# Optimization experiments

Hardware: AMD Instinct MI355X
Metric: run time of the kernel (lower is better)

## Reference

```python
import jax, jax.numpy as jnp
import numpy as np

N, D = 65536, 64            # flattened batch, state dim (size_in)
G, K = 4, 512               # number of gammas, components per gamma


def setup_inputs() -> dict:
    key = jax.random.key(0)
    k1, k2 = jax.random.split(key)
    states = jax.random.normal(k1, (N, D), dtype=jnp.float32)
    centers = jax.random.normal(k2, (G, K, D), dtype=jnp.float32)  # RBF centers, one bank per gamma
    gammas = jnp.array([0.5, 1.0, 2.0, 5.0], dtype=jnp.float32)
    return {"states": states, "centers": centers, "gammas": gammas}


def reference(states, centers, gammas):
    # states: [N, D]; centers: [G, K, D]; gammas: [G]
    x2 = jnp.sum(states * states, axis=-1)            # [N]
    c2 = jnp.sum(centers * centers, axis=-1)          # [G, K]
    xc = jnp.einsum('nd,gkd->gnk', states, centers)   # [G, N, K]
    d2 = x2[None, :, None] + c2[:, None, :] - 2.0 * xc  # [G, N, K]
    d2 = jnp.maximum(d2, 0.0)
    feats = jnp.exp(-gammas[:, None, None] * d2)      # [G, N, K]
    # concatenate per-gamma feature banks along feature dim -> [N, G*K]
    out = jnp.moveaxis(feats, 0, 1).reshape(states.shape[0], -1)
    return out
```

## Files before the change

### kernel.cpp

```cpp
#include <hip/hip_runtime.h>
#include <math.h>

#define N_TOT 65536
#define D_DIM 64
#define G_NUM 4
#define K_NUM 512
#define RB    256

typedef __attribute__((ext_vector_type(4))) float  f32x4;
typedef __attribute__((ext_vector_type(8))) short  short8;

typedef const __attribute__((address_space(1))) void glb_cv;
typedef __attribute__((address_space(3))) void lds_v;

__device__ __forceinline__ unsigned int f2u(float x)        { return __builtin_bit_cast(unsigned int, x); }
__device__ __forceinline__ float        u2f(unsigned int x) { return __builtin_bit_cast(float, x); }

__device__ __forceinline__ unsigned int bf_rne(float x) {
    unsigned int u = f2u(x);
    return (u + 0x7FFFu + ((u >> 16) & 1u)) >> 16;
}

__device__ __forceinline__ int swz(int row, int byteInRow) {
    return (row << 7) + (byteInRow ^ ((row & 7) << 4));
}

__global__ void prep_kernel(const float* __restrict__ in,
                            unsigned char* __restrict__ tiles,
                            float* __restrict__ sq, int nrows)
{
    int gtid = blockIdx.x * 256 + threadIdx.x;
    if (gtid >= nrows * 8) return;
    int row = gtid >> 3, c = gtid & 7;
    const float* p = in + (size_t)row * D_DIM + 8 * c;
    float4 v0 = *(const float4*)p;
    float4 v1 = *(const float4*)(p + 4);
    float vs[8] = {v0.x, v0.y, v0.z, v0.w, v1.x, v1.y, v1.z, v1.w};
    unsigned hi[4], lo[4];
    float s = 0.f;
    #pragma unroll
    for (int i = 0; i < 4; ++i) {
        float a = vs[2 * i], b = vs[2 * i + 1];
        s += a * a + b * b;
        unsigned ha = f2u(a) & 0xFFFF0000u, hb = f2u(b) & 0xFFFF0000u;
        hi[i] = (ha >> 16) | hb;
        lo[i] = bf_rne(a - u2f(ha)) | (bf_rne(b - u2f(hb)) << 16);
    }
    int tile = row >> 7, r = row & 127;
    int cs = c ^ (r & 7);
    unsigned char* base = tiles + (size_t)tile * 32768 + r * 128 + cs * 16;
    *(uint4*)(base)         = make_uint4(hi[0], hi[1], hi[2], hi[3]);
    *(uint4*)(base + 16384) = make_uint4(lo[0], lo[1], lo[2], lo[3]);
    s += __shfl_xor(s, 1, 64);
    s += __shfl_xor(s, 2, 64);
    s += __shfl_xor(s, 4, 64);
    if (c == 0) sq[row] = s;
}

__global__ __launch_bounds__(512, 2)
void rbf_mfma3(const unsigned char* __restrict__ Aprep,
               const unsigned char* __restrict__ Bprep,
               const float* __restrict__ gammas,
               const float* __restrict__ x2,
               const float* __restrict__ c2,
               float* __restrict__ out)
{
    __shared__ __align__(16) unsigned char lds[131072];

    const int tid  = threadIdx.x;
    const int lane = tid & 63;
    const int w    = tid >> 6;
    const int n0   = blockIdx.x * RB;

    const unsigned char* Asrc = Aprep + (size_t)blockIdx.x * 65536;
    #pragma unroll
    for (int i = 0; i < 8; ++i) {
        const int off = i * 8192 + w * 1024;
        __builtin_amdgcn_global_load_lds((glb_cv*)(Asrc + off + lane * 16),
                                         (lds_v*)(lds + off), 16, 0, 0);
    }
    #pragma unroll
    for (int i = 0; i < 4; ++i) {
        const int off = i * 8192 + w * 1024;
        __builtin_amdgcn_global_load_lds((glb_cv*)(Bprep + off + lane * 16),
                                         (lds_v*)(lds + 65536 + off), 16, 0, 0);
    }
    __syncthreads();

    const int wrow = w >> 1;
    const int wcol = w & 1;
    const int fr   = lane & 15;
    const int q    = lane >> 4;

    short8 xhi[4][2], xlo[4][2];
    #pragma unroll
    for (int ms = 0; ms < 4; ++ms) {
        const int row = wrow * 64 + ms * 16 + fr;
        const int base = (row >> 7) * 32768;
        #pragma unroll
        for (int h = 0; h < 2; ++h) {
            const int off = base + swz(row & 127, 64 * h + 16 * q);
            xhi[ms][h] = *(const short8*)(lds + off);
            xlo[ms][h] = *(const short8*)(lds + off + 16384);
        }
    }

    float x2v[4];
    #pragma unroll
    for (int ms = 0; ms < 4; ++ms)
        x2v[ms] = x2[n0 + wrow * 64 + ms * 16 + fr];

    const float4 gm = *(const float4*)gammas;

    #pragma unroll 1
    for (int t = 0; t < 16; ++t) {
        const int g  = t >> 2;
        const int kt = t & 3;
        const int bb = 65536 + (t & 1) * 32768;

        if (t < 15) {
            const unsigned char* Bsrc = Bprep + (size_t)(t + 1) * 32768;
            const int dstb = 65536 + ((t + 1) & 1) * 32768;
            #pragma unroll
            for (int i = 0; i < 4; ++i) {
                const int off = i * 8192 + w * 1024;
                __builtin_amdgcn_global_load_lds((glb_cv*)(Bsrc + off + lane * 16),
                                                 (lds_v*)(lds + dstb + off), 16, 0, 0);
            }
        }

        f32x4 acc[4][4];
        #pragma unroll
        for (int ms = 0; ms < 4; ++ms)
            #pragma unroll
            for (int ns = 0; ns < 4; ++ns)
                acc[ms][ns] = (f32x4){0.f, 0.f, 0.f, 0.f};

        #pragma unroll
        for (int ns = 0; ns < 4; ++ns) {
            const int rowc = wcol * 64 + ns * 16 + fr;
            short8 chi[2], clo[2];
            #pragma unroll
            for (int h = 0; h < 2; ++h) {
                const int off = bb + swz(rowc, 64 * h + 16 * q);
                chi[h] = *(const short8*)(lds + off);
                clo[h] = *(const short8*)(lds + off + 16384);
            }
            #pragma unroll
            for (int ms = 0; ms < 4; ++ms) {
                #pragma unroll
                for (int h = 0; h < 2; ++h) {
                    acc[ms][ns] = __builtin_amdgcn_mfma_f32_16x16x32_bf16(chi[h], xhi[ms][h], acc[ms][ns], 0, 0, 0);
                    acc[ms][ns] = __builtin_amdgcn_mfma_f32_16x16x32_bf16(chi[h], xlo[ms][h], acc[ms][ns], 0, 0, 0);
                    acc[ms][ns] = __builtin_amdgcn_mfma_f32_16x16x32_bf16(clo[h], xhi[ms][h], acc[ms][ns], 0, 0, 0);
                }
            }
        }

        const float gamma = (g == 0) ? gm.x : (g == 1) ? gm.y : (g == 2) ? gm.z : gm.w;
        const int   col0  = g * K_NUM + kt * 128 + wcol * 64;

        float c2v[4][4];
        const float* c2g = c2 + col0;
        #pragma unroll
        for (int ns = 0; ns < 4; ++ns) {
            float4 tt = *(const float4*)(c2g + ns * 16 + 4 * q);
            c2v[ns][0] = tt.x; c2v[ns][1] = tt.y; c2v[ns][2] = tt.z; c2v[ns][3] = tt.w;
        }

        #pragma unroll
        for (int ms = 0; ms < 4; ++ms) {
            const int n = n0 + wrow * 64 + ms * 16 + fr;
            const float xv = x2v[ms];
            float* rowp = out + (size_t)n * (G_NUM * K_NUM) + col0;
            #pragma unroll
            for (int ns = 0; ns < 4; ++ns) {
                float4 o;
                o.x = __expf(-gamma * fmaxf(xv + c2v[ns][0] - 2.0f * acc[ms][ns][0], 0.f));
                o.y = __expf(-gamma * fmaxf(xv + c2v[ns][1] - 2.0f * acc[ms][ns][1], 0.f));
                o.z = __expf(-gamma * fmaxf(xv + c2v[ns][2] - 2.0f * acc[ms][ns][2], 0.f));
                o.w = __expf(-gamma * fmaxf(xv + c2v[ns][3] - 2.0f * acc[ms][ns][3], 0.f));
                *(float4*)(rowp + ns * 16 + 4 * q) = o;
            }
        }

        __syncthreads();
    }
}

extern "C" void kernel_launch(void* const* d_in, const int* in_sizes, int n_in,
                              void* d_out, int out_size, void* d_ws, size_t ws_size,
                              hipStream_t stream) {
    const float* states  = (const float*)d_in[0];
    const float* centers = (const float*)d_in[1];
    const float* gammas  = (const float*)d_in[2];
    float* out = (float*)d_out;

    unsigned char* Aprep = (unsigned char*)d_ws;
    unsigned char* Bprep = Aprep + (size_t)512 * 32768;
    float* x2 = (float*)(Bprep + (size_t)16 * 32768);
    float* c2 = x2 + N_TOT;

    prep_kernel<<<(N_TOT * 8) / 256, 256, 0, stream>>>(states, Aprep, x2, N_TOT);
    prep_kernel<<<(G_NUM * K_NUM * 8) / 256, 256, 0, stream>>>(centers, Bprep, c2, G_NUM * K_NUM);

    rbf_mfma3<<<dim3(N_TOT / RB), 512, 0, stream>>>(Aprep, Bprep, gammas, x2, c2, out);
}
```

Baseline: 571.7 us.

## Pre-pack MFMA fragments in global memory and drop LDS staging

The prep kernel now writes the hi/lo bf16 operands in per-lane MFMA fragment order, so the main kernel loads its A and B fragments straight from global memory with coalesced 16-byte loads. This removes the 128 KB LDS buffer, the double-buffered async copies into it and the per-iteration barrier. The aim is to cut LDS traffic and synchronisation and to let waves run independently. In exchange, B fragments are re-read from global/L2 by every wave on every tile, with no explicit prefetch to hide that latency.

```diff
diff --git a/kernel.cpp b/kernel.cpp
--- a/kernel.cpp
+++ b/kernel.cpp
@@ -10,9 +10,6 @@
 typedef __attribute__((ext_vector_type(4))) float  f32x4;
 typedef __attribute__((ext_vector_type(8))) short  short8;
 
-typedef const __attribute__((address_space(1))) void glb_cv;
-typedef __attribute__((address_space(3))) void lds_v;
-
 __device__ __forceinline__ unsigned int f2u(float x)        { return __builtin_bit_cast(unsigned int, x); }
 __device__ __forceinline__ float        u2f(unsigned int x) { return __builtin_bit_cast(float, x); }
 
@@ -21,13 +18,9 @@
     return (u + 0x7FFFu + ((u >> 16) & 1u)) >> 16;
 }
 
-__device__ __forceinline__ int swz(int row, int byteInRow) {
-    return (row << 7) + (byteInRow ^ ((row & 7) << 4));
-}
-
-__global__ void prep_kernel(const float* __restrict__ in,
-                            unsigned char* __restrict__ tiles,
-                            float* __restrict__ sq, int nrows)
+__global__ void prep_frag_kernel(const float* __restrict__ in,
+                                 unsigned char* __restrict__ frags,
+                                 float* __restrict__ sq, int nrows, int rpt_shift)
 {
     int gtid = blockIdx.x * 256 + threadIdx.x;
     if (gtid >= nrows * 8) return;
@@ -46,11 +39,18 @@
         hi[i] = (ha >> 16) | hb;
         lo[i] = bf_rne(a - u2f(ha)) | (bf_rne(b - u2f(hb)) << 16);
     }
-    int tile = row >> 7, r = row & 127;
-    int cs = c ^ (r & 7);
-    unsigned char* base = tiles + (size_t)tile * 32768 + r * 128 + cs * 16;
-    *(uint4*)(base)         = make_uint4(hi[0], hi[1], hi[2], hi[3]);
-    *(uint4*)(base + 16384) = make_uint4(lo[0], lo[1], lo[2], lo[3]);
+    const int tile  = row >> rpt_shift;
+    const int rin   = row & ((1 << rpt_shift) - 1);
+    const int row16 = rin >> 4;
+    const int fr    = row & 15;
+    const int q     = c & 3;
+    const int h     = c >> 2;
+    const int r16s  = 1 << (rpt_shift - 4);
+    unsigned char* base = frags
+        + ((((size_t)tile * r16s + row16) * 2 + h) * 2) * 1024
+        + (size_t)(q * 16 + fr) * 16;
+    *(uint4*)(base)        = make_uint4(hi[0], hi[1], hi[2], hi[3]);
+    *(uint4*)(base + 1024) = make_uint4(lo[0], lo[1], lo[2], lo[3]);
     s += __shfl_xor(s, 1, 64);
     s += __shfl_xor(s, 2, 64);
     s += __shfl_xor(s, 4, 64);
@@ -58,50 +58,32 @@
 }
 
 __global__ __launch_bounds__(512, 2)
-void rbf_mfma3(const unsigned char* __restrict__ Aprep,
-               const unsigned char* __restrict__ Bprep,
+void rbf_mfma4(const unsigned char* __restrict__ Afrag,
+               const unsigned char* __restrict__ Bfrag,
                const float* __restrict__ gammas,
                const float* __restrict__ x2,
                const float* __restrict__ c2,
                float* __restrict__ out)
 {
-    __shared__ __align__(16) unsigned char lds[131072];
-
     const int tid  = threadIdx.x;
     const int lane = tid & 63;
     const int w    = tid >> 6;
-    const int n0   = blockIdx.x * RB;
-
-    const unsigned char* Asrc = Aprep + (size_t)blockIdx.x * 65536;
-    #pragma unroll
-    for (int i = 0; i < 8; ++i) {
-        const int off = i * 8192 + w * 1024;
-        __builtin_amdgcn_global_load_lds((glb_cv*)(Asrc + off + lane * 16),
-                                         (lds_v*)(lds + off), 16, 0, 0);
-    }
-    #pragma unroll
-    for (int i = 0; i < 4; ++i) {
-        const int off = i * 8192 + w * 1024;
-        __builtin_amdgcn_global_load_lds((glb_cv*)(Bprep + off + lane * 16),
-                                         (lds_v*)(lds + 65536 + off), 16, 0, 0);
-    }
-    __syncthreads();
-
     const int wrow = w >> 1;
     const int wcol = w & 1;
     const int fr   = lane & 15;
     const int q    = lane >> 4;
+    const int n0   = blockIdx.x * RB;
 
     short8 xhi[4][2], xlo[4][2];
+    const unsigned char* Ab = Afrag + (size_t)blockIdx.x * 65536;
     #pragma unroll
     for (int ms = 0; ms < 4; ++ms) {
-        const int row = wrow * 64 + ms * 16 + fr;
-        const int base = (row >> 7) * 32768;
         #pragma unroll
         for (int h = 0; h < 2; ++h) {
-            const int off = base + swz(row & 127, 64 * h + 16 * q);
-            xhi[ms][h] = *(const short8*)(lds + off);
-            xlo[ms][h] = *(const short8*)(lds + off + 16384);
+            const unsigned char* p = Ab + (((size_t)(wrow * 4 + ms) * 2 + h) * 2) * 1024
+                                        + (size_t)lane * 16;
+            xhi[ms][h] = *(const short8*)(p);
+            xlo[ms][h] = *(const short8*)(p + 1024);
         }
     }
 
@@ -116,18 +98,6 @@
     for (int t = 0; t < 16; ++t) {
         const int g  = t >> 2;
         const int kt = t & 3;
-        const int bb = 65536 + (t & 1) * 32768;
-
-        if (t < 15) {
-            const unsigned char* Bsrc = Bprep + (size_t)(t + 1) * 32768;
-            const int dstb = 65536 + ((t + 1) & 1) * 32768;
-            #pragma unroll
-            for (int i = 0; i < 4; ++i) {
-                const int off = i * 8192 + w * 1024;
-                __builtin_amdgcn_global_load_lds((glb_cv*)(Bsrc + off + lane * 16),
-                                                 (lds_v*)(lds + dstb + off), 16, 0, 0);
-            }
-        }
 
         f32x4 acc[4][4];
         #pragma unroll
@@ -138,13 +108,14 @@
 
         #pragma unroll
         for (int ns = 0; ns < 4; ++ns) {
-            const int rowc = wcol * 64 + ns * 16 + fr;
             short8 chi[2], clo[2];
             #pragma unroll
             for (int h = 0; h < 2; ++h) {
-                const int off = bb + swz(rowc, 64 * h + 16 * q);
-                chi[h] = *(const short8*)(lds + off);
-                clo[h] = *(const short8*)(lds + off + 16384);
+                const unsigned char* p = Bfrag
+                    + ((((size_t)t * 8 + wcol * 4 + ns) * 2 + h) * 2) * 1024
+                    + (size_t)lane * 16;
+                chi[h] = *(const short8*)(p);
+                clo[h] = *(const short8*)(p + 1024);
             }
             #pragma unroll
             for (int ms = 0; ms < 4; ++ms) {
@@ -183,8 +154,6 @@
                 *(float4*)(rowp + ns * 16 + 4 * q) = o;
             }
         }
-
-        __syncthreads();
     }
 }
 
@@ -196,13 +165,13 @@
     const float* gammas  = (const float*)d_in[2];
     float* out = (float*)d_out;
 
-    unsigned char* Aprep = (unsigned char*)d_ws;
-    unsigned char* Bprep = Aprep + (size_t)512 * 32768;
-    float* x2 = (float*)(Bprep + (size_t)16 * 32768);
+    unsigned char* Afrag = (unsigned char*)d_ws;
+    unsigned char* Bfrag = Afrag + (size_t)256 * 65536;
+    float* x2 = (float*)(Bfrag + (size_t)16 * 32768);
     float* c2 = x2 + N_TOT;
 
-    prep_kernel<<<(N_TOT * 8) / 256, 256, 0, stream>>>(states, Aprep, x2, N_TOT);
-    prep_kernel<<<(G_NUM * K_NUM * 8) / 256, 256, 0, stream>>>(centers, Bprep, c2, G_NUM * K_NUM);
+    prep_frag_kernel<<<(N_TOT * 8) / 256, 256, 0, stream>>>(states, Afrag, x2, N_TOT, 8);
+    prep_frag_kernel<<<(G_NUM * K_NUM * 8) / 256, 256, 0, stream>>>(centers, Bfrag, c2, G_NUM * K_NUM, 7);
 
-    rbf_mfma3<<<dim3(N_TOT / RB), 512, 0, stream>>>(Aprep, Bprep, gammas, x2, c2, out);
+    rbf_mfma4<<<dim3(N_TOT / RB), 512, 0, stream>>>(Afrag, Bfrag, gammas, x2, c2, out);
 }
```

Result: slower. 642.8 us (+12.4%).
